# Performance work log

Measured on AMD Instinct MI355X. Metric: run time of the kernel, lower is better.

The kernel has to match this reference:

```python
import jax, jax.numpy as jnp
import numpy as np

LENGTH = 128            # initial window length
ADJUSTED_LENGTH = 32    # stride / incremental window length
DEPTH = 2               # signature truncation depth
PATH_LEN = 262144
DIM = 64


def restricted_exp(dz, depth):
    """Tensor-algebra exponential of a single increment (levels 1..depth):
    term_k = dz^{\otimes k} / k!  (signature of one linear segment)."""
    terms = [dz]
    for k in range(2, depth + 1):
        terms.append(jnp.tensordot(terms[-1], dz, axes=0) / k)
    return tuple(terms)


def sig_combine(a, b):
    """Chen's identity: (a \otimes b)_k = a_k + b_k + sum_{i+j=k} a_i \otimes b_j."""
    depth = len(a)
    out = []
    for k in range(depth):  # level k+1
        t = a[k] + b[k]
        for i in range(k):
            t = t + jnp.tensordot(a[i], b[k - 1 - i], axes=0)
        out.append(t)
    return tuple(out)


def signature(path, depth):
    """Truncated path signature of a piecewise-linear path (L, dim)."""
    dx = path[1:] - path[:-1]  # (L-1, dim)
    init = restricted_exp(dx[0], depth)

    def step(carry, dz):
        return sig_combine(carry, restricted_exp(dz, depth)), None

    carry, _ = jax.lax.scan(step, init, dx[1:])
    return carry


def flatten_sig(sig):
    return jnp.concatenate([t.reshape(-1) for t in sig])


def setup_inputs() -> dict:
    key = jax.random.key(0)
    x = jax.random.normal(key, (PATH_LEN, DIM), dtype=jnp.float32) * 0.1
    return {"x": x}


def reference(x):
    path_len, dim = x.shape
    # window start points: length, length+adj, ... < path_len
    index = jnp.arange(LENGTH, path_len, ADJUSTED_LENGTH)

    # signature of the initial prefix
    init = signature(x[:LENGTH], DEPTH)

    # overlapping windows x[i-1 : i+adj], vectorized over all windows
    windows = jax.vmap(
        lambda i: jax.lax.dynamic_slice(x, (i - 1, 0), (ADJUSTED_LENGTH + 1, dim))
    )(index)  # (num_windows, adj+1, dim)

    # per-window signatures, vectorized (same math as computing inside the scan)
    sigs = jax.vmap(lambda w: signature(w, DEPTH))(windows)

    def step(carry, sig):
        out = sig_combine(carry, sig)
        return out, flatten_sig(out)

    _, ret = jax.lax.scan(step, init, sigs)
    return ret  # (num_windows, dim + dim^2)
```

## Files before the change

kernel.cpp:

```cpp
#include <hip/hip_runtime.h>

#define DIM 64
#define NW 8188
#define OUT_STRIDE 4160
#define NCHUNK 32

template <int WPGv, bool EMIT>
__global__ __launch_bounds__(256) void k_sweep(const float* __restrict__ x,
                                               float* __restrict__ T,
                                               const float* __restrict__ C,
                                               float* __restrict__ out) {
  __shared__ float sm[32][DIM];
  __shared__ float sd[32][DIM];
  const int g = blockIdx.x, tid = threadIdx.x;
  const int wcount = min(WPGv, NW - g * WPGv);
  const int t0 = 128 + 32 * WPGv * g;
  const int a0 = (tid >> 4) << 2, b0 = (tid & 15) << 2;
  const int a4 = b0;
  const int ti0 = tid >> 4, ti1 = ti0 + 16;
  const float4 x0v = *(const float4*)&x[a4];

  float acc[4][4];
  if (EMIT) {
    const float* Tg = T + (size_t)g * 4096;
    const float* Cc = C + (size_t)(g / NCHUNK) * 4096;
#pragma unroll
    for (int i = 0; i < 4; ++i) {
      const float4 tv = *(const float4*)&Tg[(a0 + i) * DIM + b0];
      const float4 cv = *(const float4*)&Cc[(a0 + i) * DIM + b0];
      acc[i][0] = tv.x + cv.x; acc[i][1] = tv.y + cv.y;
      acc[i][2] = tv.z + cv.z; acc[i][3] = tv.w + cv.w;
    }
  } else {
#pragma unroll
    for (int i = 0; i < 4; ++i)
      acc[i][0] = acc[i][1] = acc[i][2] = acc[i][3] = 0.f;
  }

  float4 c0, p0, c1, p1;
  auto issue = [&](int tw) {
    c0 = *(const float4*)&x[(size_t)(tw + ti0) * DIM + a4];
    p0 = *(const float4*)&x[(size_t)(tw + ti0 - 1) * DIM + a4];
    c1 = *(const float4*)&x[(size_t)(tw + ti1) * DIM + a4];
    p1 = *(const float4*)&x[(size_t)(tw + ti1 - 1) * DIM + a4];
  };
  issue(t0);

  for (int w = 0; w < wcount; ++w) {
    float4 m0, d0, m1, d1;
    m0.x = 0.5f * (c0.x + p0.x) - x0v.x; m0.y = 0.5f * (c0.y + p0.y) - x0v.y;
    m0.z = 0.5f * (c0.z + p0.z) - x0v.z; m0.w = 0.5f * (c0.w + p0.w) - x0v.w;
    d0.x = c0.x - p0.x; d0.y = c0.y - p0.y; d0.z = c0.z - p0.z; d0.w = c0.w - p0.w;
    m1.x = 0.5f * (c1.x + p1.x) - x0v.x; m1.y = 0.5f * (c1.y + p1.y) - x0v.y;
    m1.z = 0.5f * (c1.z + p1.z) - x0v.z; m1.w = 0.5f * (c1.w + p1.w) - x0v.w;
    d1.x = c1.x - p1.x; d1.y = c1.y - p1.y; d1.z = c1.z - p1.z; d1.w = c1.w - p1.w;
    if (w) __syncthreads();
    *(float4*)&sm[ti0][a4] = m0; *(float4*)&sd[ti0][a4] = d0;
    *(float4*)&sm[ti1][a4] = m1; *(float4*)&sd[ti1][a4] = d1;
    __syncthreads();
    if (w + 1 < wcount) issue(t0 + 32 * (w + 1));
#pragma unroll 8
    for (int ti = 0; ti < 32; ++ti) {
      const float4 mv = *(const float4*)&sm[ti][a0];
      const float4 dv = *(const float4*)&sd[ti][b0];
      acc[0][0] += mv.x * dv.x; acc[0][1] += mv.x * dv.y; acc[0][2] += mv.x * dv.z; acc[0][3] += mv.x * dv.w;
      acc[1][0] += mv.y * dv.x; acc[1][1] += mv.y * dv.y; acc[1][2] += mv.y * dv.z; acc[1][3] += mv.y * dv.w;
      acc[2][0] += mv.z * dv.x; acc[2][1] += mv.z * dv.y; acc[2][2] += mv.z * dv.z; acc[2][3] += mv.z * dv.w;
      acc[3][0] += mv.w * dv.x; acc[3][1] += mv.w * dv.y; acc[3][2] += mv.w * dv.z; acc[3][3] += mv.w * dv.w;
    }
    if (EMIT) {
      const int j = g * WPGv + w;
      float* row = out + (size_t)j * OUT_STRIDE;
      const int n = t0 + 32 * w + 31;
      if (tid < 64) row[tid] = x[(size_t)n * DIM + tid] - x[tid];
#pragma unroll
      for (int i = 0; i < 4; ++i)
        *(float4*)&row[64 + (a0 + i) * DIM + b0] =
            make_float4(acc[i][0], acc[i][1], acc[i][2], acc[i][3]);
    }
  }
  if (!EMIT) {
    float* Tg = T + (size_t)g * 4096;
#pragma unroll
    for (int i = 0; i < 4; ++i)
      *(float4*)&Tg[(a0 + i) * DIM + b0] =
          make_float4(acc[i][0], acc[i][1], acc[i][2], acc[i][3]);
  }
}

template <int NGv>
__global__ __launch_bounds__(256) void k_scanA(float* __restrict__ T,
                                               float* __restrict__ C) {
  const int c = blockIdx.x >> 4;
  const int e = (blockIdx.x & 15) * 256 + threadIdx.x;
  const int gbeg = c * NCHUNK, gend = min(gbeg + NCHUNK, NGv);
  float acc = 0.f;
  for (int g = gbeg; g < gend; ++g) {
    const size_t idx = (size_t)g * 4096 + e;
    const float t = T[idx];
    T[idx] = acc;
    acc += t;
  }
  C[(size_t)c * 4096 + e] = acc;
}

template <int NCv>
__global__ __launch_bounds__(256) void k_scanB(const float* __restrict__ x,
                                               float* __restrict__ C) {
  __shared__ float sx[128][DIM];
  const int tid = threadIdx.x;
  for (int f = tid; f < 128 * (DIM / 4); f += 256) {
    const int r = f >> 4, c4 = (f & 15) << 2;
    *(float4*)&sx[r][c4] = *(const float4*)&x[(size_t)r * DIM + c4];
  }
  __syncthreads();
  const int e = blockIdx.x * 256 + tid;
  const int a = e >> 6, b = e & 63;
  float acc = 0.f;
  for (int t = 1; t < 128; ++t)
    acc += (0.5f * (sx[t][a] + sx[t - 1][a]) - sx[0][a]) *
           (sx[t][b] - sx[t - 1][b]);
  for (int c = 0; c < NCv; ++c) {
    const size_t idx = (size_t)c * 4096 + e;
    const float t = C[idx];
    C[idx] = acc;
    acc += t;
  }
}

extern "C" void kernel_launch(void* const* d_in, const int* in_sizes, int n_in,
                              void* d_out, int out_size, void* d_ws, size_t ws_size,
                              hipStream_t stream) {
  const float* x = (const float*)d_in[0];
  float* out = (float*)d_out;
  const size_t need4 = (size_t)(2047 + 64) * 4096 * sizeof(float);
  if (ws_size >= need4) {
    float* T = (float*)d_ws;
    float* C = T + (size_t)2047 * 4096;
    k_sweep<4, false><<<2047, 256, 0, stream>>>(x, T, nullptr, nullptr);
    k_scanA<2047><<<64 * 16, 256, 0, stream>>>(T, C);
    k_scanB<64><<<16, 256, 0, stream>>>(x, C);
    k_sweep<4, true><<<2047, 256, 0, stream>>>(x, T, C, out);
  } else {
    float* T = (float*)d_ws;
    float* C = T + (size_t)1024 * 4096;
    k_sweep<8, false><<<1024, 256, 0, stream>>>(x, T, nullptr, nullptr);
    k_scanA<1024><<<32 * 16, 256, 0, stream>>>(T, C);
    k_scanB<32><<<16, 256, 0, stream>>>(x, C);
    k_sweep<8, true><<<1024, 256, 0, stream>>>(x, T, C, out);
  }
}
```

Measured before the change: 243.9 us.

## Assign one window group per wavefront with 8x8 register tiles and no block barriers

Each 64-lane wavefront now handles its own window group with a private LDS slice, so the block-wide __syncthreads calls go away. The per-thread outer-product tile grows from 4x4 to 8x8, which cuts LDS reads per FMA. Each wavefront prefetches the next window's rows into 16 float4 registers. The level-1 output is now rebuilt from the LDS midpoint and delta instead of re-reading x. The cost is much higher register pressure (128 accumulators plus 16 float4 prefetch registers), which may lower occupancy, and it relies on lockstep execution within a wavefront when reusing the LDS slice.

```diff
diff --git a/kernel.cpp b/kernel.cpp
--- a/kernel.cpp
+++ b/kernel.cpp
@@ -5,86 +5,113 @@
 #define OUT_STRIDE 4160
 #define NCHUNK 32
 
-template <int WPGv, bool EMIT>
+template <int WPW, int NGv, bool EMIT>
 __global__ __launch_bounds__(256) void k_sweep(const float* __restrict__ x,
                                                float* __restrict__ T,
                                                const float* __restrict__ C,
                                                float* __restrict__ out) {
-  __shared__ float sm[32][DIM];
-  __shared__ float sd[32][DIM];
-  const int g = blockIdx.x, tid = threadIdx.x;
-  const int wcount = min(WPGv, NW - g * WPGv);
-  const int t0 = 128 + 32 * WPGv * g;
-  const int a0 = (tid >> 4) << 2, b0 = (tid & 15) << 2;
-  const int a4 = b0;
-  const int ti0 = tid >> 4, ti1 = ti0 + 16;
-  const float4 x0v = *(const float4*)&x[a4];
+  __shared__ float sm[4][32][DIM];
+  __shared__ float sd[4][32][DIM];
+  const int tid = threadIdx.x, wid = tid >> 6, lane = tid & 63;
+  const int g = blockIdx.x * 4 + wid;
+  if (g >= NGv) return;
+  float(*SM)[DIM] = sm[wid];
+  float(*SD)[DIM] = sd[wid];
+  const int wcount = min(WPW, NW - g * WPW);
+  const int t0 = 128 + 32 * WPW * g;
+  const int A8 = (lane >> 3) << 3, B8 = (lane & 7) << 3;
+  const int srow = lane >> 4;
+  const int scol = (lane & 15) << 2;
+  const float4 x0q = *(const float4*)&x[scol];
 
-  float acc[4][4];
+  float4 acc[8][2];
   if (EMIT) {
     const float* Tg = T + (size_t)g * 4096;
     const float* Cc = C + (size_t)(g / NCHUNK) * 4096;
 #pragma unroll
-    for (int i = 0; i < 4; ++i) {
-      const float4 tv = *(const float4*)&Tg[(a0 + i) * DIM + b0];
-      const float4 cv = *(const float4*)&Cc[(a0 + i) * DIM + b0];
-      acc[i][0] = tv.x + cv.x; acc[i][1] = tv.y + cv.y;
-      acc[i][2] = tv.z + cv.z; acc[i][3] = tv.w + cv.w;
+    for (int i = 0; i < 8; ++i) {
+#pragma unroll
+      for (int q = 0; q < 2; ++q) {
+        const float4 tv = *(const float4*)&Tg[(A8 + i) * DIM + B8 + 4 * q];
+        const float4 cv = *(const float4*)&Cc[(A8 + i) * DIM + B8 + 4 * q];
+        acc[i][q] = make_float4(tv.x + cv.x, tv.y + cv.y, tv.z + cv.z, tv.w + cv.w);
+      }
     }
   } else {
 #pragma unroll
-    for (int i = 0; i < 4; ++i)
-      acc[i][0] = acc[i][1] = acc[i][2] = acc[i][3] = 0.f;
+    for (int i = 0; i < 8; ++i)
+#pragma unroll
+      for (int q = 0; q < 2; ++q) acc[i][q] = make_float4(0.f, 0.f, 0.f, 0.f);
   }
 
-  float4 c0, p0, c1, p1;
+  float4 rc[8], rp[8];
   auto issue = [&](int tw) {
-    c0 = *(const float4*)&x[(size_t)(tw + ti0) * DIM + a4];
-    p0 = *(const float4*)&x[(size_t)(tw + ti0 - 1) * DIM + a4];
-    c1 = *(const float4*)&x[(size_t)(tw + ti1) * DIM + a4];
-    p1 = *(const float4*)&x[(size_t)(tw + ti1 - 1) * DIM + a4];
+#pragma unroll
+    for (int j = 0; j < 8; ++j) {
+      const size_t r = (size_t)(tw + 4 * j + srow) * DIM + scol;
+      rc[j] = *(const float4*)&x[r];
+      rp[j] = *(const float4*)&x[r - DIM];
+    }
   };
   issue(t0);
 
   for (int w = 0; w < wcount; ++w) {
-    float4 m0, d0, m1, d1;
-    m0.x = 0.5f * (c0.x + p0.x) - x0v.x; m0.y = 0.5f * (c0.y + p0.y) - x0v.y;
-    m0.z = 0.5f * (c0.z + p0.z) - x0v.z; m0.w = 0.5f * (c0.w + p0.w) - x0v.w;
-    d0.x = c0.x - p0.x; d0.y = c0.y - p0.y; d0.z = c0.z - p0.z; d0.w = c0.w - p0.w;
-    m1.x = 0.5f * (c1.x + p1.x) - x0v.x; m1.y = 0.5f * (c1.y + p1.y) - x0v.y;
-    m1.z = 0.5f * (c1.z + p1.z) - x0v.z; m1.w = 0.5f * (c1.w + p1.w) - x0v.w;
-    d1.x = c1.x - p1.x; d1.y = c1.y - p1.y; d1.z = c1.z - p1.z; d1.w = c1.w - p1.w;
-    if (w) __syncthreads();
-    *(float4*)&sm[ti0][a4] = m0; *(float4*)&sd[ti0][a4] = d0;
-    *(float4*)&sm[ti1][a4] = m1; *(float4*)&sd[ti1][a4] = d1;
-    __syncthreads();
+#pragma unroll
+    for (int j = 0; j < 8; ++j) {
+      const int rr = 4 * j + srow;
+      float4 m, d;
+      m.x = 0.5f * (rc[j].x + rp[j].x) - x0q.x;
+      m.y = 0.5f * (rc[j].y + rp[j].y) - x0q.y;
+      m.z = 0.5f * (rc[j].z + rp[j].z) - x0q.z;
+      m.w = 0.5f * (rc[j].w + rp[j].w) - x0q.w;
+      d.x = rc[j].x - rp[j].x;
+      d.y = rc[j].y - rp[j].y;
+      d.z = rc[j].z - rp[j].z;
+      d.w = rc[j].w - rp[j].w;
+      *(float4*)&SM[rr][scol] = m;
+      *(float4*)&SD[rr][scol] = d;
+    }
     if (w + 1 < wcount) issue(t0 + 32 * (w + 1));
-#pragma unroll 8
+
+#pragma unroll 4
     for (int ti = 0; ti < 32; ++ti) {
-      const float4 mv = *(const float4*)&sm[ti][a0];
-      const float4 dv = *(const float4*)&sd[ti][b0];
-      acc[0][0] += mv.x * dv.x; acc[0][1] += mv.x * dv.y; acc[0][2] += mv.x * dv.z; acc[0][3] += mv.x * dv.w;
-      acc[1][0] += mv.y * dv.x; acc[1][1] += mv.y * dv.y; acc[1][2] += mv.y * dv.z; acc[1][3] += mv.y * dv.w;
-      acc[2][0] += mv.z * dv.x; acc[2][1] += mv.z * dv.y; acc[2][2] += mv.z * dv.z; acc[2][3] += mv.z * dv.w;
-      acc[3][0] += mv.w * dv.x; acc[3][1] += mv.w * dv.y; acc[3][2] += mv.w * dv.z; acc[3][3] += mv.w * dv.w;
+      const float4 m0 = *(const float4*)&SM[ti][A8];
+      const float4 m1 = *(const float4*)&SM[ti][A8 + 4];
+      const float4 d0 = *(const float4*)&SD[ti][B8];
+      const float4 d1 = *(const float4*)&SD[ti][B8 + 4];
+      const float ma[8] = {m0.x, m0.y, m0.z, m0.w, m1.x, m1.y, m1.z, m1.w};
+#pragma unroll
+      for (int i = 0; i < 8; ++i) {
+        acc[i][0].x += ma[i] * d0.x;
+        acc[i][0].y += ma[i] * d0.y;
+        acc[i][0].z += ma[i] * d0.z;
+        acc[i][0].w += ma[i] * d0.w;
+        acc[i][1].x += ma[i] * d1.x;
+        acc[i][1].y += ma[i] * d1.y;
+        acc[i][1].z += ma[i] * d1.z;
+        acc[i][1].w += ma[i] * d1.w;
+      }
     }
+
     if (EMIT) {
-      const int j = g * WPGv + w;
+      const int j = g * WPW + w;
       float* row = out + (size_t)j * OUT_STRIDE;
-      const int n = t0 + 32 * w + 31;
-      if (tid < 64) row[tid] = x[(size_t)n * DIM + tid] - x[tid];
+      row[lane] = SM[31][lane] + 0.5f * SD[31][lane];
+      float* r2 = row + 64;
 #pragma unroll
-      for (int i = 0; i < 4; ++i)
-        *(float4*)&row[64 + (a0 + i) * DIM + b0] =
-            make_float4(acc[i][0], acc[i][1], acc[i][2], acc[i][3]);
+      for (int i = 0; i < 8; ++i) {
+        *(float4*)&r2[(A8 + i) * DIM + B8] = acc[i][0];
+        *(float4*)&r2[(A8 + i) * DIM + B8 + 4] = acc[i][1];
+      }
     }
   }
   if (!EMIT) {
     float* Tg = T + (size_t)g * 4096;
 #pragma unroll
-    for (int i = 0; i < 4; ++i)
-      *(float4*)&Tg[(a0 + i) * DIM + b0] =
-          make_float4(acc[i][0], acc[i][1], acc[i][2], acc[i][3]);
+    for (int i = 0; i < 8; ++i) {
+      *(float4*)&Tg[(A8 + i) * DIM + B8] = acc[i][0];
+      *(float4*)&Tg[(A8 + i) * DIM + B8 + 4] = acc[i][1];
+    }
   }
 }
 
@@ -137,16 +164,16 @@
   if (ws_size >= need4) {
     float* T = (float*)d_ws;
     float* C = T + (size_t)2047 * 4096;
-    k_sweep<4, false><<<2047, 256, 0, stream>>>(x, T, nullptr, nullptr);
+    k_sweep<4, 2047, false><<<512, 256, 0, stream>>>(x, T, C, nullptr);
     k_scanA<2047><<<64 * 16, 256, 0, stream>>>(T, C);
     k_scanB<64><<<16, 256, 0, stream>>>(x, C);
-    k_sweep<4, true><<<2047, 256, 0, stream>>>(x, T, C, out);
+    k_sweep<4, 2047, true><<<512, 256, 0, stream>>>(x, T, C, out);
   } else {
     float* T = (float*)d_ws;
     float* C = T + (size_t)1024 * 4096;
-    k_sweep<8, false><<<1024, 256, 0, stream>>>(x, T, nullptr, nullptr);
+    k_sweep<8, 1024, false><<<256, 256, 0, stream>>>(x, T, C, nullptr);
     k_scanA<1024><<<32 * 16, 256, 0, stream>>>(T, C);
     k_scanB<32><<<16, 256, 0, stream>>>(x, C);
-    k_sweep<8, true><<<1024, 256, 0, stream>>>(x, T, C, out);
+    k_sweep<8, 1024, true><<<256, 256, 0, stream>>>(x, T, C, out);
   }
 }
```

Result: slower. 255.3 us (+4.7%).
